# Kernel optimization log

Hardware: AMD Instinct MI355X
Metric: run time of the kernel (lower is better)

Reference implementation:

```python
import jax, jax.numpy as jnp
import numpy as np

U, I, K = 20000, 10000, 64
HID = [128, 64, 32, 16]  # hidden[0] must equal 2*K
B = 4096


def _lin(key, out_f, in_f):
    # torch nn.Linear default init ~ U(-1/sqrt(in), 1/sqrt(in)); normal/sqrt(in) is fine for a baseline
    return jax.random.normal(key, (out_f, in_f), jnp.float32) / np.sqrt(in_f)


def setup_inputs() -> dict:
    key = jax.random.key(0)
    ks = jax.random.split(key, 12)
    # near-binary implicit-feedback interaction matrix [U+1, I+1]
    interactions = (jax.random.uniform(ks[0], (U + 1, I + 1)) < 0.05).astype(jnp.float32)
    user_idx = jax.random.randint(ks[1], (B,), 0, U)
    item_idx = jax.random.randint(ks[2], (B,), 0, I)
    W_u = _lin(ks[3], K, I)   # proj_u: Linear(n_items -> K, bias=False)
    W_i = _lin(ks[4], K, U)   # proj_i: Linear(n_users -> K, bias=False)
    inp = dict(interactions=interactions, user_idx=user_idx, item_idx=item_idx,
               W_u=W_u, W_i=W_i)
    # matching_fn: 3 blocks of Linear + LayerNorm (+ReLU, dropout=0 in eval)
    for j in range(1, len(HID)):
        inp[f'W{j}'] = _lin(ks[4 + j], HID[j], HID[j - 1])
        inp[f'b{j}'] = jnp.zeros((HID[j],), jnp.float32)
        inp[f'g{j}'] = jnp.ones((HID[j],), jnp.float32)
        inp[f'be{j}'] = jnp.zeros((HID[j],), jnp.float32)
    inp['Wp'] = _lin(ks[8], 1, HID[-1])
    inp['bp'] = jnp.zeros((1,), jnp.float32)
    return inp


def _layernorm(x, g, b, eps=1e-5):
    m = jnp.mean(x, axis=-1, keepdims=True)
    v = jnp.mean(jnp.square(x - m), axis=-1, keepdims=True)
    return (x - m) * jax.lax.rsqrt(v + eps) * g + b


def reference(interactions, user_idx, item_idx, W_u, W_i,
              W1, b1, g1, be1, W2, b2, g2, be2, W3, b3, g3, be3, Wp, bp):
    rows = jnp.arange(user_idx.shape[0])
    # gather user history rows [B, I], zero-mask the target item
    u_slice = interactions[user_idx, :-1].at[rows, item_idx].set(0.0)
    # gather item history rows [B, U], zero-mask the target user
    i_slice = interactions.T[item_idx, :-1].at[rows, user_idx].set(0.0)
    u_emb = u_slice @ W_u.T  # [B, K]
    i_emb = i_slice @ W_i.T  # [B, K]
    x = jnp.concatenate([u_emb, i_emb], axis=-1)  # [B, 2K]
    for (W, b, g, be) in ((W1, b1, g1, be1), (W2, b2, g2, be2), (W3, b3, g3, be3)):
        x = jax.nn.relu(_layernorm(x @ W.T + b, g, be))
    logit = jnp.squeeze(x @ Wp.T + bp, -1)  # [B]
    return logit
```

## Files before the change

kernel.cpp:

```cpp
#include <hip/hip_runtime.h>

#define U_ROWS 20000
#define I_COLS 10000
#define LDI    10001
#define B_N    4096
#define SU     313
#define SC     625

typedef __attribute__((ext_vector_type(8))) __bf16 bf16x8;
typedef __attribute__((ext_vector_type(4))) float f32x4;

__device__ __forceinline__ unsigned short f2bf(float f) {
    unsigned int u = __float_as_uint(f);
    return (unsigned short)((u + 0x7FFFu + ((u >> 16) & 1u)) >> 16);
}

__global__ __launch_bounds__(256) void k_prep(
    const float* __restrict__ Wu, const float* __restrict__ Wi,
    unsigned short* __restrict__ Pu, unsigned short* __restrict__ Pi,
    const float* __restrict__ W1, const float* __restrict__ W2, const float* __restrict__ W3,
    float* __restrict__ Wt1, float* __restrict__ Wt2, float* __restrict__ Wt3)
{
    const int NU = SU * 2048, NC2 = SC * 2048;
    int idx = blockIdx.x * 256 + threadIdx.x;
    if (idx < NU + NC2) {
        const float* W = (idx < NU) ? Wu : Wi;
        unsigned short* out = (idx < NU) ? Pu : Pi;
        int n_k = (idx < NU) ? I_COLS : U_ROWS;
        int li = (idx < NU) ? idx : idx - NU;
        int j  = li & 7;
        int l  = (li >> 3) & 63;
        int nb = (li >> 9) & 3;
        int s  = li >> 11;
        int n  = nb * 16 + (l & 15);
        int k  = s * 32 + ((l >> 4) << 3) + j;
        float v = (k < n_k) ? W[(size_t)n * n_k + k] : 0.0f;
        out[li] = f2bf(v);
        return;
    }
    int r2 = idx - (NU + NC2);
    if (r2 < 64 * 128) { int r = r2 / 128, c = r2 % 128; Wt1[c * 64 + r] = W1[r2]; return; }
    r2 -= 64 * 128;
    if (r2 < 32 * 64)  { int r = r2 / 64,  c = r2 % 64;  Wt2[c * 32 + r] = W2[r2]; return; }
    r2 -= 32 * 64;
    if (r2 < 16 * 32)  { int r = r2 / 32,  c = r2 % 32;  Wt3[c * 16 + r] = W3[r2]; return; }
}

__global__ __launch_bounds__(256) void k_gemm(
    const float* __restrict__ A, const int* __restrict__ uidx,
    const unsigned short* __restrict__ Bpu, const unsigned short* __restrict__ Bpc,
    float* __restrict__ Upart, float* __restrict__ Cpart,
    int spu, int spc, int NC)
{
    __shared__ float At[2048];
    const int t = threadIdx.x, lane = t & 63, w = t >> 6;
    const int rl = lane & 15, g = lane >> 4;
    const int CB = 157 * NC;

    f32x4 acc[4];
#pragma unroll
    for (int nb = 0; nb < 4; ++nb) acc[nb] = (f32x4)(0.0f);

    if ((int)blockIdx.x < CB) {
        const int mb = blockIdx.x % 157, p = blockIdx.x / 157;
        const int i0 = mb * 64;
        const int s0 = p * spc;
        const int s1 = (SC < s0 + spc) ? SC : (s0 + spc);

#define CLOAD(dst, S) do { \
        int u0_ = (S) * 32; \
        _Pragma("unroll") \
        for (int q = 0; q < 8; ++q) { \
            int ul_ = q * 4 + w; \
            int col_ = i0 + ((lane + ul_) & 63); \
            dst[q] = (col_ < I_COLS) ? A[(size_t)(u0_ + ul_) * LDI + col_] : 0.0f; \
        } } while (0)

        float sv[8];
        CLOAD(sv, s0);
        for (int s = s0; s < s1; ++s) {
            __syncthreads();
            float sv2[8];
            if (s + 1 < s1) { CLOAD(sv2, s + 1); }
            else {
#pragma unroll
                for (int q = 0; q < 8; ++q) sv2[q] = 0.0f;
            }
#pragma unroll
            for (int q = 0; q < 8; ++q) At[(q * 4 + w) * 64 + lane] = sv[q];

            bf16x8 bv[4];
#pragma unroll
            for (int nb = 0; nb < 4; ++nb)
                bv[nb] = *(const bf16x8*)(Bpc + ((size_t)(s * 4 + nb) * 64 + lane) * 8);
            __syncthreads();

            const int i_loc = w * 16 + rl;
            unsigned int au[8];
#pragma unroll
            for (int j = 0; j < 8; ++j) {
                int ul = g * 8 + j;
                au[j] = __float_as_uint(At[ul * 64 + ((i_loc - ul) & 63)]);
            }
            union { int i[4]; bf16x8 v; } af;
#pragma unroll
            for (int q = 0; q < 4; ++q)
                af.i[q] = __builtin_amdgcn_perm(au[2 * q + 1], au[2 * q], 0x07060302);
#pragma unroll
            for (int nb = 0; nb < 4; ++nb)
                acc[nb] = __builtin_amdgcn_mfma_f32_16x16x32_bf16(af.v, bv[nb], acc[nb], 0, 0, 0);
#pragma unroll
            for (int q = 0; q < 8; ++q) sv[q] = sv2[q];
        }

        float* outp = Cpart + (size_t)p * I_COLS * 64;
#pragma unroll
        for (int nb = 0; nb < 4; ++nb)
#pragma unroll
            for (int reg = 0; reg < 4; ++reg) {
                int i = i0 + w * 16 + g * 4 + reg;
                if (i < I_COLS) outp[(size_t)i * 64 + nb * 16 + rl] = acc[nb][reg];
            }
    } else {
        const int bid = blockIdx.x - CB;
        const int mb = bid & 63, p = bid >> 6;
        const int r0 = mb * 64;
        const int s0 = p * spu;
        const int s1 = (SU < s0 + spu) ? SU : (s0 + spu);

        int urow[8];
#pragma unroll
        for (int q = 0; q < 8; ++q) urow[q] = uidx[r0 + q * 8 + (t >> 5)];

#define ULOAD(dst, S) do { \
        int k0_ = (S) * 32; \
        _Pragma("unroll") \
        for (int q = 0; q < 8; ++q) { \
            int row_ = q * 8 + (t >> 5); \
            int col_ = k0_ + (((t & 31) + row_) & 31); \
            dst[q] = (col_ < I_COLS) ? A[(size_t)urow[q] * LDI + col_] : 0.0f; \
        } } while (0)

        float sv[8];
        ULOAD(sv, s0);
        for (int s = s0; s < s1; ++s) {
            __syncthreads();
            float sv2[8];
            if (s + 1 < s1) { ULOAD(sv2, s + 1); }
            else {
#pragma unroll
                for (int q = 0; q < 8; ++q) sv2[q] = 0.0f;
            }
#pragma unroll
            for (int q = 0; q < 8; ++q) {
                int row = q * 8 + (t >> 5);
                At[row * 32 + (t & 31)] = sv[q];
            }
            bf16x8 bv[4];
#pragma unroll
            for (int nb = 0; nb < 4; ++nb)
                bv[nb] = *(const bf16x8*)(Bpu + ((size_t)(s * 4 + nb) * 64 + lane) * 8);
            __syncthreads();

            const int r_loc = w * 16 + rl;
            unsigned int au[8];
#pragma unroll
            for (int j = 0; j < 8; ++j) {
                int c = g * 8 + j;
                au[j] = __float_as_uint(At[r_loc * 32 + ((c - r_loc) & 31)]);
            }
            union { int i[4]; bf16x8 v; } af;
#pragma unroll
            for (int q = 0; q < 4; ++q)
                af.i[q] = __builtin_amdgcn_perm(au[2 * q + 1], au[2 * q], 0x07060302);
#pragma unroll
            for (int nb = 0; nb < 4; ++nb)
                acc[nb] = __builtin_amdgcn_mfma_f32_16x16x32_bf16(af.v, bv[nb], acc[nb], 0, 0, 0);
#pragma unroll
            for (int q = 0; q < 8; ++q) sv[q] = sv2[q];
        }

        float* outp = Upart + (size_t)p * B_N * 64;
#pragma unroll
        for (int nb = 0; nb < 4; ++nb)
#pragma unroll
            for (int reg = 0; reg < 4; ++reg) {
                int r = r0 + w * 16 + g * 4 + reg;
                outp[(size_t)r * 64 + nb * 16 + rl] = acc[nb][reg];
            }
    }
}

__device__ __forceinline__ float redsum64(float x) {
    x += __shfl_xor(x, 1);  x += __shfl_xor(x, 2);  x += __shfl_xor(x, 4);
    x += __shfl_xor(x, 8);  x += __shfl_xor(x, 16); x += __shfl_xor(x, 32);
    return x;
}
__device__ __forceinline__ float redsum32(float x) {
    x += __shfl_xor(x, 1); x += __shfl_xor(x, 2); x += __shfl_xor(x, 4);
    x += __shfl_xor(x, 8); x += __shfl_xor(x, 16);
    return x;
}
__device__ __forceinline__ float redsum16(float x) {
    x += __shfl_xor(x, 1); x += __shfl_xor(x, 2); x += __shfl_xor(x, 4);
    x += __shfl_xor(x, 8);
    return x;
}

__global__ __launch_bounds__(256) void k_epi(
    const float* __restrict__ A, const int* __restrict__ uidx, const int* __restrict__ iidx,
    const float* __restrict__ Upart, const float* __restrict__ Cpart, int NP, int NC,
    const float* __restrict__ Wu, const float* __restrict__ Wi,
    const float* __restrict__ Wt1, const float* __restrict__ b1, const float* __restrict__ g1, const float* __restrict__ be1,
    const float* __restrict__ Wt2, const float* __restrict__ b2, const float* __restrict__ g2, const float* __restrict__ be2,
    const float* __restrict__ Wt3, const float* __restrict__ b3, const float* __restrict__ g3, const float* __restrict__ be3,
    const float* __restrict__ Wp, const float* __restrict__ bp,
    float* __restrict__ out)
{
    const int t = threadIdx.x, lane = t & 63, w = t >> 6;
    const int r = blockIdx.x * 4 + w;
    const int u = uidx[r], it = iidx[r];
    const float a_ui = A[(size_t)u * LDI + it];

    float ue = 0.f, ie = 0.f;
    for (int p0 = 0; p0 < NP; ++p0) ue += Upart[((size_t)p0 * B_N + r) * 64 + lane];
    for (int p0 = 0; p0 < NC; ++p0) ie += Cpart[((size_t)p0 * I_COLS + it) * 64 + lane];
    ue -= a_ui * Wu[(size_t)lane * I_COLS + it];
    ie -= a_ui * Wi[(size_t)lane * U_ROWS + u];

    float h = b1[lane];
    for (int c = 0; c < 64; ++c) h += __shfl(ue, c) * Wt1[c * 64 + lane];
    for (int c = 0; c < 64; ++c) h += __shfl(ie, c) * Wt1[(64 + c) * 64 + lane];
    {
        float m = redsum64(h) * (1.0f / 64.0f);
        float d = h - m;
        float v = redsum64(d * d) * (1.0f / 64.0f);
        h = d * rsqrtf(v + 1e-5f) * g1[lane] + be1[lane];
        h = fmaxf(h, 0.0f);
    }
    const int l2 = lane & 31;
    float h2 = b2[l2];
    for (int c = 0; c < 64; ++c) h2 += __shfl(h, c) * Wt2[c * 32 + l2];
    {
        float m = redsum32(h2) * (1.0f / 32.0f);
        float d = h2 - m;
        float v = redsum32(d * d) * (1.0f / 32.0f);
        h2 = d * rsqrtf(v + 1e-5f) * g2[l2] + be2[l2];
        h2 = fmaxf(h2, 0.0f);
    }
    const int l3 = lane & 15;
    float h3 = b3[l3];
    for (int c = 0; c < 32; ++c) h3 += __shfl(h2, c) * Wt3[c * 16 + l3];
    {
        float m = redsum16(h3) * (1.0f / 16.0f);
        float d = h3 - m;
        float v = redsum16(d * d) * (1.0f / 16.0f);
        h3 = d * rsqrtf(v + 1e-5f) * g3[l3] + be3[l3];
        h3 = fmaxf(h3, 0.0f);
    }
    float tt = h3 * Wp[l3];
    tt = redsum16(tt);
    if (lane == 0) out[r] = tt + bp[0];
}

extern "C" void kernel_launch(void* const* d_in, const int* in_sizes, int n_in,
                              void* d_out, int out_size, void* d_ws, size_t ws_size,
                              hipStream_t stream)
{
    const float* A    = (const float*)d_in[0];
    const int*   uidx = (const int*)d_in[1];
    const int*   iidx = (const int*)d_in[2];
    const float* W_u  = (const float*)d_in[3];
    const float* W_i  = (const float*)d_in[4];
    const float* W1   = (const float*)d_in[5];
    const float* b1   = (const float*)d_in[6];
    const float* g1   = (const float*)d_in[7];
    const float* be1  = (const float*)d_in[8];
    const float* W2   = (const float*)d_in[9];
    const float* b2   = (const float*)d_in[10];
    const float* g2   = (const float*)d_in[11];
    const float* be2  = (const float*)d_in[12];
    const float* W3   = (const float*)d_in[13];
    const float* b3   = (const float*)d_in[14];
    const float* g3   = (const float*)d_in[15];
    const float* be3  = (const float*)d_in[16];
    const float* Wp   = (const float*)d_in[17];
    const float* bp   = (const float*)d_in[18];
    float* out = (float*)d_out;

    unsigned short* Wtu_p = (unsigned short*)d_ws;
    unsigned short* Wti_p = Wtu_p + (size_t)SU * 2048;
    float* Wt1 = (float*)(Wti_p + (size_t)SC * 2048);
    float* Wt2 = Wt1 + 128 * 64;
    float* Wt3 = Wt2 + 64 * 32;
    float* Upart = Wt3 + 32 * 16;

    size_t fixed_b = (size_t)(SU + SC) * 2048 * 2 + (size_t)(128 * 64 + 64 * 32 + 32 * 16) * 4;
    int NP = 8, NC = 8;
    while (NP > 1 &&
           fixed_b + (size_t)NP * B_N * 64 * 4 + (size_t)NC * I_COLS * 64 * 4 > ws_size) {
        NP >>= 1; NC >>= 1;
    }
    float* Cpart = Upart + (size_t)NP * B_N * 64;

    int spu = (SU + NP - 1) / NP;
    int spc = (SC + NC - 1) / NC;

    int prep_tot = (SU + SC) * 2048 + 64 * 128 + 32 * 64 + 16 * 32;
    hipLaunchKernelGGL(k_prep, dim3((prep_tot + 255) / 256), dim3(256), 0, stream,
                       W_u, W_i, Wtu_p, Wti_p, W1, W2, W3, Wt1, Wt2, Wt3);

    hipLaunchKernelGGL(k_gemm, dim3(157 * NC + 64 * NP), dim3(256), 0, stream,
                       A, uidx, Wtu_p, Wti_p, Upart, Cpart, spu, spc, NC);

    hipLaunchKernelGGL(k_epi, dim3(B_N / 4), dim3(256), 0, stream,
                       A, uidx, iidx, Upart, Cpart, NP, NC,
                       W_u, W_i, Wt1, b1, g1, be1, Wt2, b2, g2, be2,
                       Wt3, b3, g3, be3, Wp, bp, out);
}
```

Before: 250.4 us.

## Load A directly into MFMA fragments, drop LDS staging, pre-transpose embedding weights

```diff
diff --git a/kernel.cpp b/kernel.cpp
--- a/kernel.cpp
+++ b/kernel.cpp
@@ -19,7 +19,8 @@
     const float* __restrict__ Wu, const float* __restrict__ Wi,
     unsigned short* __restrict__ Pu, unsigned short* __restrict__ Pi,
     const float* __restrict__ W1, const float* __restrict__ W2, const float* __restrict__ W3,
-    float* __restrict__ Wt1, float* __restrict__ Wt2, float* __restrict__ Wt3)
+    float* __restrict__ Wt1, float* __restrict__ Wt2, float* __restrict__ Wt3,
+    float* __restrict__ WuT, float* __restrict__ WiT)
 {
     const int NU = SU * 2048, NC2 = SC * 2048;
     int idx = blockIdx.x * 256 + threadIdx.x;
@@ -44,6 +45,18 @@
     if (r2 < 32 * 64)  { int r = r2 / 64,  c = r2 % 64;  Wt2[c * 32 + r] = W2[r2]; return; }
     r2 -= 32 * 64;
     if (r2 < 16 * 32)  { int r = r2 / 32,  c = r2 % 32;  Wt3[c * 16 + r] = W3[r2]; return; }
+    r2 -= 16 * 32;
+    if (r2 < 64 * I_COLS) {
+        int n = r2 / I_COLS, k = r2 % I_COLS;
+        WuT[(size_t)k * 64 + n] = Wu[r2];
+        return;
+    }
+    r2 -= 64 * I_COLS;
+    if (r2 < 64 * U_ROWS) {
+        int n = r2 / U_ROWS, u = r2 % U_ROWS;
+        WiT[(size_t)u * 64 + n] = Wi[r2];
+        return;
+    }
 }
 
 __global__ __launch_bounds__(256) void k_gemm(
@@ -52,65 +65,58 @@
     float* __restrict__ Upart, float* __restrict__ Cpart,
     int spu, int spc, int NC)
 {
-    __shared__ float At[2048];
     const int t = threadIdx.x, lane = t & 63, w = t >> 6;
     const int rl = lane & 15, g = lane >> 4;
     const int CB = 157 * NC;
+    const char* Ab = (const char*)A;
 
     f32x4 acc[4];
 #pragma unroll
     for (int nb = 0; nb < 4; ++nb) acc[nb] = (f32x4)(0.0f);
 
     if ((int)blockIdx.x < CB) {
-        const int mb = blockIdx.x % 157, p = blockIdx.x / 157;
+        const int p = blockIdx.x % NC, mb = blockIdx.x / NC;
         const int i0 = mb * 64;
+        const int ci = i0 + w * 16 + rl;
+        const int ci_eff = (ci < I_COLS) ? ci : 0;
         const int s0 = p * spc;
         const int s1 = (SC < s0 + spc) ? SC : (s0 + spc);
 
-#define CLOAD(dst, S) do { \
-        int u0_ = (S) * 32; \
+        unsigned int off[8];
+#pragma unroll
+        for (int j = 0; j < 8; ++j)
+            off[j] = (unsigned int)(((s0 * 32 + g * 8 + j) * LDI + ci_eff) * 4);
+
+#define CLOADP(dst) do { \
         _Pragma("unroll") \
-        for (int q = 0; q < 8; ++q) { \
-            int ul_ = q * 4 + w; \
-            int col_ = i0 + ((lane + ul_) & 63); \
-            dst[q] = (col_ < I_COLS) ? A[(size_t)(u0_ + ul_) * LDI + col_] : 0.0f; \
+        for (int j_ = 0; j_ < 8; ++j_) { \
+            dst[j_] = *(const float*)(Ab + off[j_]); \
+            off[j_] += 32u * LDI * 4u; \
         } } while (0)
 
-        float sv[8];
-        CLOAD(sv, s0);
+        float av[8];
+        CLOADP(av);
         for (int s = s0; s < s1; ++s) {
-            __syncthreads();
-            float sv2[8];
-            if (s + 1 < s1) { CLOAD(sv2, s + 1); }
+            float nx[8];
+            if (s + 1 < s1) { CLOADP(nx); }
             else {
 #pragma unroll
-                for (int q = 0; q < 8; ++q) sv2[q] = 0.0f;
+                for (int j = 0; j < 8; ++j) nx[j] = 0.0f;
             }
-#pragma unroll
-            for (int q = 0; q < 8; ++q) At[(q * 4 + w) * 64 + lane] = sv[q];
-
             bf16x8 bv[4];
 #pragma unroll
             for (int nb = 0; nb < 4; ++nb)
                 bv[nb] = *(const bf16x8*)(Bpc + ((size_t)(s * 4 + nb) * 64 + lane) * 8);
-            __syncthreads();
-
-            const int i_loc = w * 16 + rl;
-            unsigned int au[8];
-#pragma unroll
-            for (int j = 0; j < 8; ++j) {
-                int ul = g * 8 + j;
-                au[j] = __float_as_uint(At[ul * 64 + ((i_loc - ul) & 63)]);
-            }
             union { int i[4]; bf16x8 v; } af;
 #pragma unroll
             for (int q = 0; q < 4; ++q)
-                af.i[q] = __builtin_amdgcn_perm(au[2 * q + 1], au[2 * q], 0x07060302);
+                af.i[q] = __builtin_amdgcn_perm(__float_as_uint(av[2 * q + 1]),
+                                                __float_as_uint(av[2 * q]), 0x07060302);
 #pragma unroll
             for (int nb = 0; nb < 4; ++nb)
                 acc[nb] = __builtin_amdgcn_mfma_f32_16x16x32_bf16(af.v, bv[nb], acc[nb], 0, 0, 0);
 #pragma unroll
-            for (int q = 0; q < 8; ++q) sv[q] = sv2[q];
+            for (int j = 0; j < 8; ++j) av[j] = nx[j];
         }
 
         float* outp = Cpart + (size_t)p * I_COLS * 64;
@@ -123,61 +129,44 @@
             }
     } else {
         const int bid = blockIdx.x - CB;
-        const int mb = bid & 63, p = bid >> 6;
+        const int p = bid % NC, mb = bid / NC;
         const int r0 = mb * 64;
         const int s0 = p * spu;
         const int s1 = (SU < s0 + spu) ? SU : (s0 + spu);
 
-        int urow[8];
-#pragma unroll
-        for (int q = 0; q < 8; ++q) urow[q] = uidx[r0 + q * 8 + (t >> 5)];
-
-#define ULOAD(dst, S) do { \
-        int k0_ = (S) * 32; \
-        _Pragma("unroll") \
-        for (int q = 0; q < 8; ++q) { \
-            int row_ = q * 8 + (t >> 5); \
-            int col_ = k0_ + (((t & 31) + row_) & 31); \
-            dst[q] = (col_ < I_COLS) ? A[(size_t)urow[q] * LDI + col_] : 0.0f; \
-        } } while (0)
-
-        float sv[8];
-        ULOAD(sv, s0);
+        const int ur = uidx[r0 + w * 16 + rl];
+        unsigned int offu = (unsigned int)(((size_t)ur * LDI + s0 * 32 + g * 8) * 4);
+
+        union F8 { float f[8]; f32x4 v[2]; };
+#define ULOADP(dst, S) do { \
+        int kb_ = (S) * 32 + g * 8; \
+        dst.v[0] = (kb_     < I_COLS) ? *(const f32x4*)(Ab + offu)      : (f32x4)(0.0f); \
+        dst.v[1] = (kb_ + 4 < I_COLS) ? *(const f32x4*)(Ab + offu + 16) : (f32x4)(0.0f); \
+        offu += 128u; } while (0)
+
+        F8 av;
+        ULOADP(av, s0);
         for (int s = s0; s < s1; ++s) {
-            __syncthreads();
-            float sv2[8];
-            if (s + 1 < s1) { ULOAD(sv2, s + 1); }
+            F8 nx;
+            if (s + 1 < s1) { ULOADP(nx, s + 1); }
             else {
 #pragma unroll
-                for (int q = 0; q < 8; ++q) sv2[q] = 0.0f;
-            }
-#pragma unroll
-            for (int q = 0; q < 8; ++q) {
-                int row = q * 8 + (t >> 5);
-                At[row * 32 + (t & 31)] = sv[q];
+                for (int j = 0; j < 8; ++j) nx.f[j] = 0.0f;
             }
             bf16x8 bv[4];
 #pragma unroll
             for (int nb = 0; nb < 4; ++nb)
                 bv[nb] = *(const bf16x8*)(Bpu + ((size_t)(s * 4 + nb) * 64 + lane) * 8);
-            __syncthreads();
-
-            const int r_loc = w * 16 + rl;
-            unsigned int au[8];
-#pragma unroll
-            for (int j = 0; j < 8; ++j) {
-                int c = g * 8 + j;
-                au[j] = __float_as_uint(At[r_loc * 32 + ((c - r_loc) & 31)]);
-            }
             union { int i[4]; bf16x8 v; } af;
 #pragma unroll
             for (int q = 0; q < 4; ++q)
-                af.i[q] = __builtin_amdgcn_perm(au[2 * q + 1], au[2 * q], 0x07060302);
+                af.i[q] = __builtin_amdgcn_perm(__float_as_uint(av.f[2 * q + 1]),
+                                                __float_as_uint(av.f[2 * q]), 0x07060302);
 #pragma unroll
             for (int nb = 0; nb < 4; ++nb)
                 acc[nb] = __builtin_amdgcn_mfma_f32_16x16x32_bf16(af.v, bv[nb], acc[nb], 0, 0, 0);
 #pragma unroll
-            for (int q = 0; q < 8; ++q) sv[q] = sv2[q];
+            for (int j = 0; j < 8; ++j) av.f[j] = nx.f[j];
         }
 
         float* outp = Upart + (size_t)p * B_N * 64;
@@ -210,7 +199,7 @@
 __global__ __launch_bounds__(256) void k_epi(
     const float* __restrict__ A, const int* __restrict__ uidx, const int* __restrict__ iidx,
     const float* __restrict__ Upart, const float* __restrict__ Cpart, int NP, int NC,
-    const float* __restrict__ Wu, const float* __restrict__ Wi,
+    const float* __restrict__ WuT, const float* __restrict__ WiT,
     const float* __restrict__ Wt1, const float* __restrict__ b1, const float* __restrict__ g1, const float* __restrict__ be1,
     const float* __restrict__ Wt2, const float* __restrict__ b2, const float* __restrict__ g2, const float* __restrict__ be2,
     const float* __restrict__ Wt3, const float* __restrict__ b3, const float* __restrict__ g3, const float* __restrict__ be3,
@@ -225,8 +214,8 @@
     float ue = 0.f, ie = 0.f;
     for (int p0 = 0; p0 < NP; ++p0) ue += Upart[((size_t)p0 * B_N + r) * 64 + lane];
     for (int p0 = 0; p0 < NC; ++p0) ie += Cpart[((size_t)p0 * I_COLS + it) * 64 + lane];
-    ue -= a_ui * Wu[(size_t)lane * I_COLS + it];
-    ie -= a_ui * Wi[(size_t)lane * U_ROWS + u];
+    ue -= a_ui * WuT[(size_t)it * 64 + lane];
+    ie -= a_ui * WiT[(size_t)u * 64 + lane];
 
     float h = b1[lane];
     for (int c = 0; c < 64; ++c) h += __shfl(ue, c) * Wt1[c * 64 + lane];
@@ -293,9 +282,13 @@
     float* Wt1 = (float*)(Wti_p + (size_t)SC * 2048);
     float* Wt2 = Wt1 + 128 * 64;
     float* Wt3 = Wt2 + 64 * 32;
-    float* Upart = Wt3 + 32 * 16;
-
-    size_t fixed_b = (size_t)(SU + SC) * 2048 * 2 + (size_t)(128 * 64 + 64 * 32 + 32 * 16) * 4;
+    float* WuT = Wt3 + 32 * 16;
+    float* WiT = WuT + (size_t)I_COLS * 64;
+    float* Upart = WiT + (size_t)U_ROWS * 64;
+
+    size_t fixed_b = (size_t)(SU + SC) * 2048 * 2
+                   + (size_t)(128 * 64 + 64 * 32 + 32 * 16) * 4
+                   + (size_t)(I_COLS + U_ROWS) * 64 * 4;
     int NP = 8, NC = 8;
     while (NP > 1 &&
            fixed_b + (size_t)NP * B_N * 64 * 4 + (size_t)NC * I_COLS * 64 * 4 > ws_size) {
@@ -306,15 +299,16 @@
     int spu = (SU + NP - 1) / NP;
     int spc = (SC + NC - 1) / NC;
 
-    int prep_tot = (SU + SC) * 2048 + 64 * 128 + 32 * 64 + 16 * 32;
+    int prep_tot = (SU + SC) * 2048 + 64 * 128 + 32 * 64 + 16 * 32
+                 + 64 * I_COLS + 64 * U_ROWS;
     hipLaunchKernelGGL(k_prep, dim3((prep_tot + 255) / 256), dim3(256), 0, stream,
-                       W_u, W_i, Wtu_p, Wti_p, W1, W2, W3, Wt1, Wt2, Wt3);
+                       W_u, W_i, Wtu_p, Wti_p, W1, W2, W3, Wt1, Wt2, Wt3, WuT, WiT);
 
     hipLaunchKernelGGL(k_gemm, dim3(157 * NC + 64 * NP), dim3(256), 0, stream,
                        A, uidx, Wtu_p, Wti_p, Upart, Cpart, spu, spc, NC);
 
     hipLaunchKernelGGL(k_epi, dim3(B_N / 4), dim3(256), 0, stream,
                        A, uidx, iidx, Upart, Cpart, NP, NC,
-                       W_u, W_i, Wt1, b1, g1, be1, Wt2, b2, g2, be2,
+                       WuT, WiT, Wt1, b1, g1, be1, Wt2, b2, g2, be2,
                        Wt3, b3, g3, be3, Wp, bp, out);
 }
```

New measurement: 344.6 us. +37.6%, slower.
